# Kernel optimization log

Measured on AMD Instinct MI355X. Metric: run time of the kernel, lower is better.

Reference implementation:

```python
import jax, jax.numpy as jnp
import numpy as np

C0 = 32        # num_feat_maps[0]
LD = 6         # latent_dim
NC = 1         # num_classes
B, P = 1, 96


def setup_inputs() -> dict:
    key = jax.random.key(0)
    ks = jax.random.split(key, 10)
    s = lambda fan_in: 1.0 / np.sqrt(fan_in)
    return {
        "feature_map": jax.random.normal(ks[0], (B, C0, P, P, P), dtype=jnp.float32),
        "z": jax.random.normal(ks[1], (B, LD), dtype=jnp.float32),
        "w1": jax.random.normal(ks[2], (C0, C0 + LD), dtype=jnp.float32) * s(C0 + LD),
        "b1": jnp.zeros((C0,), dtype=jnp.float32),
        "w2": jax.random.normal(ks[3], (C0, C0), dtype=jnp.float32) * s(C0),
        "b2": jnp.zeros((C0,), dtype=jnp.float32),
        "w3": jax.random.normal(ks[4], (C0, C0), dtype=jnp.float32) * s(C0),
        "b3": jnp.zeros((C0,), dtype=jnp.float32),
        "wl": jax.random.normal(ks[5], (NC, C0), dtype=jnp.float32) * s(C0),
        "bl": jnp.zeros((NC,), dtype=jnp.float32),
    }


def _pw(x, w, b):
    # 1x1x1 conv3d == pointwise channel GEMM: [B,Ci,X,Y,Z] x [Co,Ci] -> [B,Co,X,Y,Z]
    return jnp.einsum('bcxyz,oc->boxyz', x, w) + b[None, :, None, None, None]


def reference(feature_map, z, w1, b1, w2, b2, w3, b3, wl, bl):
    b, _, x_, y_, z_ = feature_map.shape
    # tile() on the unsqueezed z is equivalent to broadcasting over spatial dims
    zb = jnp.broadcast_to(z[:, :, None, None, None], (b, z.shape[1], x_, y_, z_))
    h = jnp.concatenate([feature_map, zb], axis=1)          # [B, C0+LD, P,P,P]
    h = jax.nn.relu(_pw(h, w1, b1))
    h = jax.nn.relu(_pw(h, w2, b2))
    h = jax.nn.relu(_pw(h, w3, b3))
    return _pw(h, wl, bl)                                    # [B, NC, P,P,P]
```

## Files before the change

### kernel.cpp

```cpp
#include <hip/hip_runtime.h>


typedef float    f32x16 __attribute__((ext_vector_type(16)));
typedef short    bf16x8 __attribute__((ext_vector_type(8)));
typedef unsigned u32x4  __attribute__((ext_vector_type(4)));

constexpr int NPTS  = 96 * 96 * 96;
constexpr int TILE  = 512;
constexpr int BLOCK = 256;
constexpr int NBLK  = NPTS / TILE;

typedef __attribute__((address_space(1))) const void glob_void;
typedef __attribute__((address_space(3))) void lds_void;

__device__ __forceinline__ unsigned cvtpk(float lo, float hi) {
    unsigned d;
    asm("v_cvt_pk_bf16_f32 %0, %1, %2" : "=v"(d) : "v"(lo), "v"(hi));
    return d;
}
__device__ __forceinline__ float unlo(unsigned d) { return __uint_as_float(d << 16); }

__device__ __forceinline__ bf16x8 mk4(unsigned a, unsigned b, unsigned c, unsigned d) {
    u32x4 u; u.x = a; u.y = b; u.z = c; u.w = d;
    return __builtin_bit_cast(bf16x8, u);
}

__device__ __forceinline__ void swap32(unsigned a, unsigned b, unsigned& x, unsigned& y) {
    auto r = __builtin_amdgcn_permlane32_swap(a, b, false, false);
    x = r[0]; y = r[1];
}

__device__ __forceinline__ void load_wsplit(const float* __restrict__ W, int stride,
                                            int row, int koff, bf16x8& Hf, bf16x8& Lf) {
    const float2* p2 = reinterpret_cast<const float2*>(W + row * stride + koff);
    float2 q0 = p2[0], q1 = p2[1], q2 = p2[2], q3 = p2[3];
    unsigned h0 = cvtpk(q0.x, q0.y), h1 = cvtpk(q1.x, q1.y);
    unsigned h2 = cvtpk(q2.x, q2.y), h3 = cvtpk(q3.x, q3.y);
    unsigned l0 = cvtpk(q0.x - unlo(h0), q0.y - __uint_as_float(h0 & 0xffff0000u));
    unsigned l1 = cvtpk(q1.x - unlo(h1), q1.y - __uint_as_float(h1 & 0xffff0000u));
    unsigned l2 = cvtpk(q2.x - unlo(h2), q2.y - __uint_as_float(h2 & 0xffff0000u));
    unsigned l3 = cvtpk(q3.x - unlo(h3), q3.y - __uint_as_float(h3 & 0xffff0000u));
    Hf = mk4(h0, h1, h2, h3);
    Lf = mk4(l0, l1, l2, l3);
}

__device__ __forceinline__ void pack_frags(const f32x16 acc, bf16x8& F0, bf16x8& F1) {
    unsigned p0 = cvtpk(fmaxf(acc[0],  0.f), fmaxf(acc[1],  0.f));
    unsigned p1 = cvtpk(fmaxf(acc[2],  0.f), fmaxf(acc[3],  0.f));
    unsigned p2 = cvtpk(fmaxf(acc[4],  0.f), fmaxf(acc[5],  0.f));
    unsigned p3 = cvtpk(fmaxf(acc[6],  0.f), fmaxf(acc[7],  0.f));
    unsigned p4 = cvtpk(fmaxf(acc[8],  0.f), fmaxf(acc[9],  0.f));
    unsigned p5 = cvtpk(fmaxf(acc[10], 0.f), fmaxf(acc[11], 0.f));
    unsigned p6 = cvtpk(fmaxf(acc[12], 0.f), fmaxf(acc[13], 0.f));
    unsigned p7 = cvtpk(fmaxf(acc[14], 0.f), fmaxf(acc[15], 0.f));
    unsigned a0, a1, b0, b1, c0, c1, d0, d1;
    swap32(p0, p2, a0, a1); swap32(p1, p3, b0, b1);
    swap32(p4, p6, c0, c1); swap32(p5, p7, d0, d1);
    F0 = mk4(a0, b0, a1, b1);
    F1 = mk4(c0, d0, c1, d1);
}

__device__ __forceinline__ unsigned bias_word(float b) {
    float bhi = unlo(cvtpk(b, b));
    return cvtpk(b, b - bhi);
}

#define WLAYER(acc, WH0, WL0, WH1, WL1, F0, F1)                                   \
    acc = __builtin_amdgcn_mfma_f32_32x32x16_bf16(WH0, F0, acc, 0, 0, 0);         \
    acc = __builtin_amdgcn_mfma_f32_32x32x16_bf16(WL0, F0, acc, 0, 0, 0);         \
    acc = __builtin_amdgcn_mfma_f32_32x32x16_bf16(WH1, F1, acc, 0, 0, 0);         \
    acc = __builtin_amdgcn_mfma_f32_32x32x16_bf16(WL1, F1, acc, 0, 0, 0);

__global__ __launch_bounds__(BLOCK, 2)
void fused_mlp_mfma(const float* __restrict__ fm, const float* __restrict__ z,
                    const float* __restrict__ w1, const float* __restrict__ b1,
                    const float* __restrict__ w2, const float* __restrict__ b2,
                    const float* __restrict__ w3, const float* __restrict__ b3,
                    const float* __restrict__ wl, const float* __restrict__ bl,
                    float* __restrict__ out)
{
    __shared__ float lds[32][TILE];

    const int lane = threadIdx.x & 63;
    const int w    = threadIdx.x >> 6;
    const int hl   = lane >> 5;
    const int col  = lane & 31;
    const int koff = 8 * hl;
    const int tb   = blockIdx.x * TILE;

    #pragma unroll
    for (int i = 0; i < 16; ++i) {
        const int idx = w * 16 + i;
        const int c   = idx >> 1;
        const int h   = idx & 1;
        const float* gsrc = fm + c * NPTS + tb + h * 256 + lane * 4;
        __builtin_amdgcn_global_load_lds((glob_void*)gsrc,
                                         (lds_void*)&lds[c][h * 256],
                                         16, 0, 0);
    }

    bf16x8 W1h0, W1l0, W1h1, W1l1, W2h0, W2l0, W2h1, W2l1, W3h0, W3l0, W3h1, W3l1;
    load_wsplit(w1, 38, col, 0  + koff, W1h0, W1l0);
    load_wsplit(w1, 38, col, 16 + koff, W1h1, W1l1);
    load_wsplit(w2, 32, col, 0  + koff, W2h0, W2l0);
    load_wsplit(w2, 32, col, 16 + koff, W2h1, W2l1);
    load_wsplit(w3, 32, col, 0  + koff, W3h0, W3l0);
    load_wsplit(w3, 32, col, 16 + koff, W3h1, W3l1);

    float b1e = b1[col];
    b1e = fmaf(w1[col * 38 + 32], z[0], b1e);
    b1e = fmaf(w1[col * 38 + 33], z[1], b1e);
    b1e = fmaf(w1[col * 38 + 34], z[2], b1e);
    b1e = fmaf(w1[col * 38 + 35], z[3], b1e);
    b1e = fmaf(w1[col * 38 + 36], z[4], b1e);
    b1e = fmaf(w1[col * 38 + 37], z[5], b1e);
    const unsigned zero = 0u;
    bf16x8 Ab1  = mk4(hl ? zero : bias_word(b1e),     zero, zero, zero);
    bf16x8 Ab2  = mk4(hl ? zero : bias_word(b2[col]), zero, zero, zero);
    bf16x8 Ab3  = mk4(hl ? zero : bias_word(b3[col]), zero, zero, zero);
    bf16x8 Bone = mk4(hl ? zero : 0x3F803F80u,        zero, zero, zero);

    f32x16 wlr;
    #pragma unroll
    for (int r = 0; r < 16; ++r) wlr[r] = wl[(r & 3) + 8 * (r >> 2) + 4 * hl];
    const float blv = bl[0];

    f32x16 zacc;
    #pragma unroll
    for (int r = 0; r < 16; ++r) zacc[r] = 0.f;

    __syncthreads();

    #pragma unroll
    for (int g = 0; g < 4; ++g) {
        const int pl = (w * 4 + g) * 32 + col;

        float v0  = lds[koff + 0][pl],  v1  = lds[koff + 1][pl];
        float v2  = lds[koff + 2][pl],  v3  = lds[koff + 3][pl];
        float v4  = lds[koff + 4][pl],  v5  = lds[koff + 5][pl];
        float v6  = lds[koff + 6][pl],  v7  = lds[koff + 7][pl];
        float v8  = lds[16 + koff + 0][pl], v9  = lds[16 + koff + 1][pl];
        float v10 = lds[16 + koff + 2][pl], v11 = lds[16 + koff + 3][pl];
        float v12 = lds[16 + koff + 4][pl], v13 = lds[16 + koff + 5][pl];
        float v14 = lds[16 + koff + 6][pl], v15 = lds[16 + koff + 7][pl];

        bf16x8 F0 = mk4(cvtpk(v0, v1),  cvtpk(v2, v3),
                        cvtpk(v4, v5),  cvtpk(v6, v7));
        bf16x8 F1 = mk4(cvtpk(v8, v9),  cvtpk(v10, v11),
                        cvtpk(v12, v13), cvtpk(v14, v15));

        f32x16 acc = __builtin_amdgcn_mfma_f32_32x32x16_bf16(Ab1, Bone, zacc, 0, 0, 0);
        WLAYER(acc, W1h0, W1l0, W1h1, W1l1, F0, F1)

        pack_frags(acc, F0, F1);
        acc = __builtin_amdgcn_mfma_f32_32x32x16_bf16(Ab2, Bone, zacc, 0, 0, 0);
        WLAYER(acc, W2h0, W2l0, W2h1, W2l1, F0, F1)

        pack_frags(acc, F0, F1);
        acc = __builtin_amdgcn_mfma_f32_32x32x16_bf16(Ab3, Bone, zacc, 0, 0, 0);
        WLAYER(acc, W3h0, W3l0, W3h1, W3l1, F0, F1)

        float s = 0.f;
        #pragma unroll
        for (int r = 0; r < 16; ++r) s = fmaf(wlr[r], fmaxf(acc[r], 0.f), s);
        unsigned px, py;
        swap32(__float_as_uint(s), __float_as_uint(s), px, py);
        float tot = __uint_as_float(px) + __uint_as_float(py) + blv;
        if (lane < 32) out[tb + pl] = tot;
    }
}

extern "C" void kernel_launch(void* const* d_in, const int* in_sizes, int n_in,
                              void* d_out, int out_size, void* d_ws, size_t ws_size,
                              hipStream_t stream)
{
    const float* fm = (const float*)d_in[0];
    const float* z  = (const float*)d_in[1];
    const float* w1 = (const float*)d_in[2];
    const float* b1 = (const float*)d_in[3];
    const float* w2 = (const float*)d_in[4];
    const float* b2 = (const float*)d_in[5];
    const float* w3 = (const float*)d_in[6];
    const float* b3 = (const float*)d_in[7];
    const float* wl = (const float*)d_in[8];
    const float* bl = (const float*)d_in[9];
    float* out = (float*)d_out;

    fused_mlp_mfma<<<NBLK, BLOCK, 0, stream>>>(
        fm, z, w1, b1, w2, b2, w3, b3, wl, bl, out);
}
```

Before: 187.5 us.

## Double-buffer LDS tiles so each block prefetches the next tile while computing

```diff
diff --git a/kernel.cpp b/kernel.cpp
--- a/kernel.cpp
+++ b/kernel.cpp
@@ -6,9 +6,10 @@
 typedef unsigned u32x4  __attribute__((ext_vector_type(4)));
 
 constexpr int NPTS  = 96 * 96 * 96;
-constexpr int TILE  = 512;
+constexpr int TILE  = 256;
+constexpr int NT    = 4;
 constexpr int BLOCK = 256;
-constexpr int NBLK  = NPTS / TILE;
+constexpr int NBLK  = NPTS / (TILE * NT);
 
 typedef __attribute__((address_space(1))) const void glob_void;
 typedef __attribute__((address_space(3))) void lds_void;
@@ -79,24 +80,21 @@
                     const float* __restrict__ wl, const float* __restrict__ bl,
                     float* __restrict__ out)
 {
-    __shared__ float lds[32][TILE];
+    __shared__ float lds[2][32][TILE];
 
     const int lane = threadIdx.x & 63;
     const int w    = threadIdx.x >> 6;
     const int hl   = lane >> 5;
     const int col  = lane & 31;
     const int koff = 8 * hl;
-    const int tb   = blockIdx.x * TILE;
-
-    #pragma unroll
-    for (int i = 0; i < 16; ++i) {
-        const int idx = w * 16 + i;
-        const int c   = idx >> 1;
-        const int h   = idx & 1;
-        const float* gsrc = fm + c * NPTS + tb + h * 256 + lane * 4;
-        __builtin_amdgcn_global_load_lds((glob_void*)gsrc,
-                                         (lds_void*)&lds[c][h * 256],
-                                         16, 0, 0);
+    const int rot  = blockIdx.x & 31;
+    const int base = blockIdx.x * (TILE * NT);
+
+    #pragma unroll
+    for (int i = 0; i < 8; ++i) {
+        const int c = (w * 8 + i + rot) & 31;
+        __builtin_amdgcn_global_load_lds((glob_void*)(fm + c * NPTS + base + lane * 4),
+                                         (lds_void*)&lds[0][c][0], 16, 0, 0);
     }
 
     bf16x8 W1h0, W1l0, W1h1, W1l1, W2h0, W2l0, W2h1, W2l1, W3h0, W3l0, W3h1, W3l1;
@@ -132,41 +130,58 @@
     __syncthreads();
 
     #pragma unroll
-    for (int g = 0; g < 4; ++g) {
-        const int pl = (w * 4 + g) * 32 + col;
-
-        float v0  = lds[koff + 0][pl],  v1  = lds[koff + 1][pl];
-        float v2  = lds[koff + 2][pl],  v3  = lds[koff + 3][pl];
-        float v4  = lds[koff + 4][pl],  v5  = lds[koff + 5][pl];
-        float v6  = lds[koff + 6][pl],  v7  = lds[koff + 7][pl];
-        float v8  = lds[16 + koff + 0][pl], v9  = lds[16 + koff + 1][pl];
-        float v10 = lds[16 + koff + 2][pl], v11 = lds[16 + koff + 3][pl];
-        float v12 = lds[16 + koff + 4][pl], v13 = lds[16 + koff + 5][pl];
-        float v14 = lds[16 + koff + 6][pl], v15 = lds[16 + koff + 7][pl];
-
-        bf16x8 F0 = mk4(cvtpk(v0, v1),  cvtpk(v2, v3),
-                        cvtpk(v4, v5),  cvtpk(v6, v7));
-        bf16x8 F1 = mk4(cvtpk(v8, v9),  cvtpk(v10, v11),
-                        cvtpk(v12, v13), cvtpk(v14, v15));
-
-        f32x16 acc = __builtin_amdgcn_mfma_f32_32x32x16_bf16(Ab1, Bone, zacc, 0, 0, 0);
-        WLAYER(acc, W1h0, W1l0, W1h1, W1l1, F0, F1)
-
-        pack_frags(acc, F0, F1);
-        acc = __builtin_amdgcn_mfma_f32_32x32x16_bf16(Ab2, Bone, zacc, 0, 0, 0);
-        WLAYER(acc, W2h0, W2l0, W2h1, W2l1, F0, F1)
-
-        pack_frags(acc, F0, F1);
-        acc = __builtin_amdgcn_mfma_f32_32x32x16_bf16(Ab3, Bone, zacc, 0, 0, 0);
-        WLAYER(acc, W3h0, W3l0, W3h1, W3l1, F0, F1)
-
-        float s = 0.f;
+    for (int t = 0; t < NT; ++t) {
+        const int cur = t & 1;
+
+        if (t + 1 < NT) {
+            const int tb2 = base + (t + 1) * TILE;
+            #pragma unroll
+            for (int i = 0; i < 8; ++i) {
+                const int c = (w * 8 + i + rot) & 31;
+                __builtin_amdgcn_global_load_lds((glob_void*)(fm + c * NPTS + tb2 + lane * 4),
+                                                 (lds_void*)&lds[cur ^ 1][c][0], 16, 0, 0);
+            }
+        }
+
         #pragma unroll
-        for (int r = 0; r < 16; ++r) s = fmaf(wlr[r], fmaxf(acc[r], 0.f), s);
-        unsigned px, py;
-        swap32(__float_as_uint(s), __float_as_uint(s), px, py);
-        float tot = __uint_as_float(px) + __uint_as_float(py) + blv;
-        if (lane < 32) out[tb + pl] = tot;
+        for (int g = 0; g < 2; ++g) {
+            const int pl = (w * 2 + g) * 32 + col;
+
+            float v0  = lds[cur][koff + 0][pl],  v1  = lds[cur][koff + 1][pl];
+            float v2  = lds[cur][koff + 2][pl],  v3  = lds[cur][koff + 3][pl];
+            float v4  = lds[cur][koff + 4][pl],  v5  = lds[cur][koff + 5][pl];
+            float v6  = lds[cur][koff + 6][pl],  v7  = lds[cur][koff + 7][pl];
+            float v8  = lds[cur][16 + koff + 0][pl], v9  = lds[cur][16 + koff + 1][pl];
+            float v10 = lds[cur][16 + koff + 2][pl], v11 = lds[cur][16 + koff + 3][pl];
+            float v12 = lds[cur][16 + koff + 4][pl], v13 = lds[cur][16 + koff + 5][pl];
+            float v14 = lds[cur][16 + koff + 6][pl], v15 = lds[cur][16 + koff + 7][pl];
+
+            bf16x8 F0 = mk4(cvtpk(v0, v1),  cvtpk(v2, v3),
+                            cvtpk(v4, v5),  cvtpk(v6, v7));
+            bf16x8 F1 = mk4(cvtpk(v8, v9),  cvtpk(v10, v11),
+                            cvtpk(v12, v13), cvtpk(v14, v15));
+
+            f32x16 acc = __builtin_amdgcn_mfma_f32_32x32x16_bf16(Ab1, Bone, zacc, 0, 0, 0);
+            WLAYER(acc, W1h0, W1l0, W1h1, W1l1, F0, F1)
+
+            pack_frags(acc, F0, F1);
+            acc = __builtin_amdgcn_mfma_f32_32x32x16_bf16(Ab2, Bone, zacc, 0, 0, 0);
+            WLAYER(acc, W2h0, W2l0, W2h1, W2l1, F0, F1)
+
+            pack_frags(acc, F0, F1);
+            acc = __builtin_amdgcn_mfma_f32_32x32x16_bf16(Ab3, Bone, zacc, 0, 0, 0);
+            WLAYER(acc, W3h0, W3l0, W3h1, W3l1, F0, F1)
+
+            float s = 0.f;
+            #pragma unroll
+            for (int r = 0; r < 16; ++r) s = fmaf(wlr[r], fmaxf(acc[r], 0.f), s);
+            unsigned px, py;
+            swap32(__float_as_uint(s), __float_as_uint(s), px, py);
+            float tot = __uint_as_float(px) + __uint_as_float(py) + blv;
+            if (lane < 32) out[base + t * TILE + pl] = tot;
+        }
+
+        __syncthreads();
     }
 }
 
```

Result: faster. 180.4 us (-3.8%).
